# Kernel tuning notes

Measured on AMD Instinct MI355X. Metric: run time of the kernel, lower is better.

## Reference

```python
import jax, jax.numpy as jnp
import numpy as np

B, T, N_EMBED = 16, 4096, 48
HEAD_SIZE, DIM = 8, 64  # dim = 2**n_wires, n_wires = 6


def setup_inputs() -> dict:
    key = jax.random.key(0)
    k1, k2, k3 = jax.random.split(key, 3)
    x = jax.random.normal(k1, (B, T, N_EMBED), dtype=jnp.float32)
    obs_re = jax.random.normal(k2, (HEAD_SIZE, DIM, DIM), dtype=jnp.float32)
    obs_im = jax.random.normal(k3, (HEAD_SIZE, DIM, DIM), dtype=jnp.float32)
    return {"x": x, "obs_re": obs_re, "obs_im": obs_im}


def reference(x, obs_re, obs_im):
    # x: (B, T, C) real; obs: (H, dim, dim) complex observables O'.
    b, t, c = x.shape
    h, dim, _ = obs_re.shape
    O = (obs_re + 1j * obs_im).astype(jnp.complex64)  # (h, dim, dim)
    # psi: zero-padded complex state, x loaded into first n_embed amplitudes
    psi = jnp.zeros((b * t, dim), dtype=jnp.complex64)
    psi = psi.at[:, :c].set(x.reshape(b * t, c).astype(jnp.complex64))
    # O_psi[h, n, i] = sum_j O[h, i, j] * psi[n, j]  (all heads in one batched GEMM)
    O_psi = jnp.einsum('hij,nj->hni', O, psi)
    # exp[n, h] = Re( psi^H O' psi )
    exp = jnp.einsum('ni,hni->nh', jnp.conj(psi), O_psi).real
    return exp.reshape(b, t, h).astype(jnp.float32)
```

## Files before the change

kernel.cpp:

```cpp
#include <hip/hip_runtime.h>


#define NTOK 65536
#define NHEAD 8
#define XSTRIDE 56
#define TPB 128

typedef __attribute__((ext_vector_type(8))) short short8;
typedef __attribute__((ext_vector_type(4))) short short4v;
typedef __attribute__((ext_vector_type(4))) float float4v;

static __device__ __forceinline__ short f2bf(float f) {
    unsigned int u = __builtin_bit_cast(unsigned int, f);
    u += 0x7FFFu + ((u >> 16) & 1u);
    return (short)(u >> 16);
}
static __device__ __forceinline__ float bf2f(short s) {
    return __builtin_bit_cast(float, ((unsigned int)(unsigned short)s) << 16);
}

__global__ __launch_bounds__(256, 2) void qform_fused(
    const float* __restrict__ x,
    const float* __restrict__ obs,
    float* __restrict__ out)
{
    __shared__ short a_lds[48 * 64 * 8];
    __shared__ short xl[TPB * XSTRIDE];

    const int tid  = threadIdx.x;
    const int w    = tid >> 6, lane = tid & 63;
    const int q    = lane >> 4, c = lane & 15;
    const int tb   = blockIdx.x * TPB;

    #pragma unroll
    for (int u = 0; u < 12; ++u) {
        int f = u * 4 + w;
        int h = f / 6, rem = f % 6, kt = rem / 3, it = rem % 3;
        const float4* src = (const float4*)(obs +
            ((size_t)(h * 64 + 16 * it + c) * 64 + 32 * kt + 8 * q));
        float4 v0 = src[0], v1 = src[1];
        short8 a;
        a[0] = f2bf(v0.x); a[1] = f2bf(v0.y); a[2] = f2bf(v0.z); a[3] = f2bf(v0.w);
        a[4] = f2bf(v1.x); a[5] = f2bf(v1.y); a[6] = f2bf(v1.z); a[7] = f2bf(v1.w);
        *(short8*)(a_lds + ((size_t)f * 64 + lane) * 8) = a;
    }

    #pragma unroll
    for (int s = 0; s < 6; ++s) {
        int idx = s * 256 + tid;
        int t = idx / 12, ch = idx % 12;
        float4 v = ((const float4*)x)[(size_t)tb * 12 + idx];
        short4v b;
        b.x = f2bf(v.x); b.y = f2bf(v.y); b.z = f2bf(v.z); b.w = f2bf(v.w);
        *(short4v*)(xl + t * XSTRIDE + ch * 4) = b;
    }
    __syncthreads();

    short8 bfr[2][2];
    float  xe[2][3][4];
    #pragma unroll
    for (int g = 0; g < 2; ++g) {
        const int row = w * 32 + g * 16 + c;
        bfr[g][0] = *(const short8*)(xl + row * XSTRIDE + q * 8);
        if (q < 2)
            bfr[g][1] = *(const short8*)(xl + row * XSTRIDE + 32 + q * 8);
        else
            bfr[g][1] = (short8)0;
        #pragma unroll
        for (int it = 0; it < 3; ++it)
            #pragma unroll
            for (int r = 0; r < 4; ++r)
                xe[g][it][r] = bf2f(xl[row * XSTRIDE + 16 * it + 4 * q + r]);
    }

    float ph[2][NHEAD];
    #pragma unroll
    for (int h = 0; h < NHEAD; ++h) {
        short8 A[6];
        #pragma unroll
        for (int u = 0; u < 6; ++u)
            A[u] = *(const short8*)(a_lds + ((size_t)(h * 6 + u) * 64 + lane) * 8);
        #pragma unroll
        for (int g = 0; g < 2; ++g) {
            float4v acc[3];
            #pragma unroll
            for (int it = 0; it < 3; ++it) {
                float4v z = {0.f, 0.f, 0.f, 0.f};
                acc[it] = __builtin_amdgcn_mfma_f32_16x16x32_bf16(A[it],     bfr[g][0], z,       0, 0, 0);
                acc[it] = __builtin_amdgcn_mfma_f32_16x16x32_bf16(A[3 + it], bfr[g][1], acc[it], 0, 0, 0);
            }
            float p = 0.f;
            #pragma unroll
            for (int it = 0; it < 3; ++it)
                #pragma unroll
                for (int r = 0; r < 4; ++r)
                    p += acc[it][r] * xe[g][it][r];
            p += __shfl_xor(p, 16, 64);
            p += __shfl_xor(p, 32, 64);
            ph[g][h] = p;
        }
    }

    if (lane < 16) {
        #pragma unroll
        for (int g = 0; g < 2; ++g) {
            float4* o4 = (float4*)(out + (size_t)(tb + w * 32 + g * 16 + c) * NHEAD);
            o4[0] = make_float4(ph[g][0], ph[g][1], ph[g][2], ph[g][3]);
            o4[1] = make_float4(ph[g][4], ph[g][5], ph[g][6], ph[g][7]);
        }
    }
}

extern "C" void kernel_launch(void* const* d_in, const int* in_sizes, int n_in,
                              void* d_out, int out_size, void* d_ws, size_t ws_size,
                              hipStream_t stream) {
    const float* x      = (const float*)d_in[0];
    const float* obs_re = (const float*)d_in[1];
    float* out = (float*)d_out;

    qform_fused<<<NTOK / TPB, 256, 0, stream>>>(x, obs_re, out);
}
```

Baseline: 71.36 us.

## Precompute bf16 observable fragments in a prep kernel and split heads across waves

Adds a small prep kernel that converts the observable matrices to bf16 MFMA fragment layout once into workspace, so each main block only copies ready fragments into LDS instead of reloading and converting fp32. The main kernel also reassigns work so each wave handles 4 heads over 64 tokens rather than 8 heads over 32 tokens, halving A-fragment LDS reads per wave while doubling the x fragments held in registers. The cost is an extra kernel launch and higher register pressure, which could lower occupancy.

```diff
diff --git a/kernel.cpp b/kernel.cpp
--- a/kernel.cpp
+++ b/kernel.cpp
@@ -19,9 +19,28 @@
     return __builtin_bit_cast(float, ((unsigned int)(unsigned short)s) << 16);
 }
 
-__global__ __launch_bounds__(256, 2) void qform_fused(
+__global__ void prep_frags(const float* __restrict__ obs, short* __restrict__ frags) {
+    const int tid  = threadIdx.x;
+    const int w    = tid >> 6, lane = tid & 63;
+    const int q    = lane >> 4, c = lane & 15;
+    const int h    = blockIdx.x * 4 + w;
+    #pragma unroll
+    for (int u = 0; u < 6; ++u) {
+        const int kt = u / 3, it = u % 3;
+        const int f  = h * 6 + u;
+        const float4* src = (const float4*)(obs +
+            ((size_t)(h * 64 + 16 * it + c) * 64 + 32 * kt + 8 * q));
+        float4 v0 = src[0], v1 = src[1];
+        short8 a;
+        a[0] = f2bf(v0.x); a[1] = f2bf(v0.y); a[2] = f2bf(v0.z); a[3] = f2bf(v0.w);
+        a[4] = f2bf(v1.x); a[5] = f2bf(v1.y); a[6] = f2bf(v1.z); a[7] = f2bf(v1.w);
+        *(short8*)(frags + ((size_t)f * 64 + lane) * 8) = a;
+    }
+}
+
+__global__ __launch_bounds__(256, 2) void qform_main(
+    const short* __restrict__ frags,
     const float* __restrict__ x,
-    const float* __restrict__ obs,
     float* __restrict__ out)
 {
     __shared__ short a_lds[48 * 64 * 8];
@@ -34,14 +53,8 @@
 
     #pragma unroll
     for (int u = 0; u < 12; ++u) {
-        int f = u * 4 + w;
-        int h = f / 6, rem = f % 6, kt = rem / 3, it = rem % 3;
-        const float4* src = (const float4*)(obs +
-            ((size_t)(h * 64 + 16 * it + c) * 64 + 32 * kt + 8 * q));
-        float4 v0 = src[0], v1 = src[1];
-        short8 a;
-        a[0] = f2bf(v0.x); a[1] = f2bf(v0.y); a[2] = f2bf(v0.z); a[3] = f2bf(v0.w);
-        a[4] = f2bf(v1.x); a[5] = f2bf(v1.y); a[6] = f2bf(v1.z); a[7] = f2bf(v1.w);
+        const int f = u * 4 + w;
+        short8 a = *(const short8*)(frags + ((size_t)f * 64 + lane) * 8);
         *(short8*)(a_lds + ((size_t)f * 64 + lane) * 8) = a;
     }
 
@@ -56,11 +69,14 @@
     }
     __syncthreads();
 
-    short8 bfr[2][2];
-    float  xe[2][3][4];
+    const int hbase = (w >> 1) * 4;
+    const int gbase = (w & 1) * 4;
+
+    short8 bfr[4][2];
+    float  xe[4][3][4];
     #pragma unroll
-    for (int g = 0; g < 2; ++g) {
-        const int row = w * 32 + g * 16 + c;
+    for (int g = 0; g < 4; ++g) {
+        const int row = (gbase + g) * 16 + c;
         bfr[g][0] = *(const short8*)(xl + row * XSTRIDE + q * 8);
         if (q < 2)
             bfr[g][1] = *(const short8*)(xl + row * XSTRIDE + 32 + q * 8);
@@ -73,15 +89,16 @@
                 xe[g][it][r] = bf2f(xl[row * XSTRIDE + 16 * it + 4 * q + r]);
     }
 
-    float ph[2][NHEAD];
+    float ph[4][4];
     #pragma unroll
-    for (int h = 0; h < NHEAD; ++h) {
+    for (int hh = 0; hh < 4; ++hh) {
+        const int h = hbase + hh;
         short8 A[6];
         #pragma unroll
         for (int u = 0; u < 6; ++u)
             A[u] = *(const short8*)(a_lds + ((size_t)(h * 6 + u) * 64 + lane) * 8);
         #pragma unroll
-        for (int g = 0; g < 2; ++g) {
+        for (int g = 0; g < 4; ++g) {
             float4v acc[3];
             #pragma unroll
             for (int it = 0; it < 3; ++it) {
@@ -97,16 +114,16 @@
                     p += acc[it][r] * xe[g][it][r];
             p += __shfl_xor(p, 16, 64);
             p += __shfl_xor(p, 32, 64);
-            ph[g][h] = p;
+            ph[g][hh] = p;
         }
     }
 
     if (lane < 16) {
         #pragma unroll
-        for (int g = 0; g < 2; ++g) {
-            float4* o4 = (float4*)(out + (size_t)(tb + w * 32 + g * 16 + c) * NHEAD);
+        for (int g = 0; g < 4; ++g) {
+            float4* o4 = (float4*)(out +
+                (size_t)(tb + (gbase + g) * 16 + c) * NHEAD + hbase);
             o4[0] = make_float4(ph[g][0], ph[g][1], ph[g][2], ph[g][3]);
-            o4[1] = make_float4(ph[g][4], ph[g][5], ph[g][6], ph[g][7]);
         }
     }
 }
@@ -116,7 +133,9 @@
                               hipStream_t stream) {
     const float* x      = (const float*)d_in[0];
     const float* obs_re = (const float*)d_in[1];
-    float* out = (float*)d_out;
+    float* out   = (float*)d_out;
+    short* frags = (short*)d_ws;
 
-    qform_fused<<<NTOK / TPB, 256, 0, stream>>>(x, obs_re, out);
+    prep_frags<<<2, 256, 0, stream>>>(obs_re, frags);
+    qform_main<<<NTOK / TPB, 256, 0, stream>>>(frags, x, out);
 }
```

Result: faster. 69.34 us (-2.8%).
